# Kernel tuning notes

Measured on AMD Instinct MI355X. Metric: run time of the kernel, lower is better.

## Reference

```python
import jax, jax.numpy as jnp
import numpy as np

B, T, D = 8, 2048, 128        # batch, time, input_dim
C, CD = 8192, 128             # codebook_size, codebook_dim
COMMIT_W = 1.0                # commitment_weight
IN2Q_W = 0.25                 # input_to_quantize_commit_loss_weight
EPS = 1e-12


def setup_inputs() -> dict:
    key = jax.random.key(0)
    k = jax.random.split(key, 4)
    z = jax.random.normal(k[0], (B, T, D), jnp.float32)
    frozen_codebook = jax.random.normal(k[1], (C, CD), jnp.float32) * CD ** -0.5
    conv_v = jax.random.normal(k[2], (D, CD), jnp.float32) * CD ** -0.5  # weight-norm direction (1x1 conv weight squeezed)
    conv_g = jnp.linalg.norm(conv_v, axis=1)                             # weight-norm gain (torch init: g = ||v||)
    conv_b = jnp.zeros((D,), jnp.float32)
    return {"z": z, "frozen_codebook": frozen_codebook, "conv_v": conv_v,
            "conv_g": conv_g, "conv_b": conv_b}


def _implicit_codebook(fc, v, g, b):
    # weight-normed 1x1 conv == linear: w = g * v / ||v||_row ; out = fc @ w.T + b
    w = g[:, None] * v / jnp.linalg.norm(v, axis=1, keepdims=True)
    return fc @ w.T + b  # (C, D)


def _rotate_to(src, tgt):
    # rotation trick (Fifty et al.): Householder-style rotation, grads flow only through src
    sg = jax.lax.stop_gradient
    norm_src = jnp.linalg.norm(src, axis=-1, keepdims=True)
    norm_tgt = jnp.linalg.norm(tgt, axis=-1, keepdims=True)
    u = sg(src / jnp.maximum(norm_src, EPS))
    q = sg(tgt / jnp.maximum(norm_tgt, EPS))
    w = u + q
    w = sg(w / jnp.maximum(jnp.linalg.norm(w, axis=-1, keepdims=True), EPS))
    e = src
    rotated = (e
               - 2.0 * jnp.sum(e * w, -1, keepdims=True) * w
               + 2.0 * jnp.sum(e * u, -1, keepdims=True) * q)
    scale = sg(norm_tgt / jnp.maximum(norm_src, EPS))
    return rotated * scale


def reference(z, frozen_codebook, conv_v, conv_g, conv_b):
    sg = jax.lax.stop_gradient
    cb = _implicit_codebook(frozen_codebook, conv_v, conv_g, conv_b)  # (C, D)
    # squared euclidean distances -> same argmin as torch.cdist (p=2)
    d2 = (jnp.sum(z * z, -1, keepdims=True)
          - 2.0 * jnp.einsum('btd,cd->btc', z, cb)
          + jnp.sum(cb * cb, -1))                                     # (B, T, C)
    indices = jnp.argmin(d2, axis=-1)                                 # (B, T)
    z_q = cb[indices]                                                 # (B, T, D)
    commit = (jnp.mean((sg(z) - z_q) ** 2)
              + IN2Q_W * jnp.mean((z - sg(z_q)) ** 2))
    z_q = _rotate_to(z, z_q)
    return z_q, indices, commit * COMMIT_W
```

## Files before the change

kernel.cpp:

```cpp
#include <hip/hip_runtime.h>
#include <math.h>

#define NROWS 16384
#define DIM 128
#define NCODE 8192
#define EPSF 1e-12f

typedef float f32x4 __attribute__((ext_vector_type(4)));
typedef __bf16 bf16x8 __attribute__((ext_vector_type(8)));
typedef unsigned short u16x8 __attribute__((ext_vector_type(8)));

#define WS_NEED_BYTES 31571968ull

#define KT 12
#define TILE 4096

__device__ __forceinline__ float wave_sum(float x) {
#pragma unroll
  for (int off = 32; off > 0; off >>= 1) x += __shfl_xor(x, off, 64);
  return x;
}

__device__ __forceinline__ unsigned short f2bf(float x) {
  union { float f; unsigned int u; } v;
  v.f = x;
  unsigned int r = v.u + 0x7fffu + ((v.u >> 16) & 1u);
  return (unsigned short)(r >> 16);
}
__device__ __forceinline__ float bf2f(unsigned short h) {
  union { float f; unsigned int u; } v;
  v.u = ((unsigned int)h) << 16;
  return v.f;
}

__device__ __forceinline__ void gload_lds16(const unsigned short* g,
                                            unsigned short* l) {
  __builtin_amdgcn_global_load_lds(
      (const __attribute__((address_space(1))) void*)g,
      (__attribute__((address_space(3))) void*)l, 16, 0, 0);
}

__global__ void wprep_kernel(const float* __restrict__ v,
                             const float* __restrict__ g,
                             float* __restrict__ Wt) {
  const int d = blockIdx.x;
  const int lane = threadIdx.x;
  const float v0 = v[d * DIM + lane], v1 = v[d * DIM + lane + 64];
  const float ss = wave_sum(fmaf(v0, v0, v1 * v1));
  const float sc = g[d] / sqrtf(ss);
  Wt[lane * DIM + d] = v0 * sc;
  Wt[(lane + 64) * DIM + d] = v1 * sc;
}

__global__ __launch_bounds__(256, 2) void codebook_kernel(
    const float* __restrict__ fc, const float* __restrict__ Wt,
    const float* __restrict__ bias, float* __restrict__ cb,
    float* __restrict__ cnorm2, unsigned short* __restrict__ cbcat) {
  __shared__ float Ws[DIM][DIM];
  const int tid = threadIdx.x;
  for (int i = tid; i < 4096; i += 256)
    *(float4*)&Ws[0][i << 2] = *(const float4*)&Wt[i << 2];
  __syncthreads();

  const int lane = tid & 63, wid = tid >> 6;
  const int c0 = blockIdx.x * 16 + wid * 4;
  const float b0 = bias[lane], b1 = bias[lane + 64];

  for (int cc = 0; cc < 4; ++cc) {
    const int c = __builtin_amdgcn_readfirstlane(c0 + cc);
    float a0 = 0.f, a1 = 0.f;
    for (int k = 0; k < DIM; k += 4) {
      const float4 f4 = *(const float4*)&fc[c * DIM + k];
      a0 = fmaf(f4.x, Ws[k][lane], a0);
      a1 = fmaf(f4.x, Ws[k][lane + 64], a1);
      a0 = fmaf(f4.y, Ws[k + 1][lane], a0);
      a1 = fmaf(f4.y, Ws[k + 1][lane + 64], a1);
      a0 = fmaf(f4.z, Ws[k + 2][lane], a0);
      a1 = fmaf(f4.z, Ws[k + 2][lane + 64], a1);
      a0 = fmaf(f4.w, Ws[k + 3][lane], a0);
      a1 = fmaf(f4.w, Ws[k + 3][lane + 64], a1);
    }
    const float o0 = a0 + b0, o1 = a1 + b1;
    cb[c * DIM + lane] = o0;
    cb[c * DIM + lane + 64] = o1;
    const float ss = wave_sum(fmaf(o0, o0, o1 * o1));
    if (lane == 0) cnorm2[c] = ss;

    if (cbcat != nullptr) {
      const int ct = c >> 7, r = c & 127;
      const unsigned int swz = ((r >> 1) & 3) << 3;
      unsigned short* base = cbcat + (size_t)ct * (KT * TILE);
#pragma unroll
      for (int h = 0; h < 2; ++h) {
        const int d = lane + 64 * h;
        const float val = h ? o1 : o0;
        const unsigned short hi = f2bf(val);
        const unsigned short lo = f2bf(val - bf2f(hi));
        const int ktl = d >> 5;
        const int off = (r << 5) + ((d & 31) ^ swz);
        base[ktl * TILE + off] = hi;
        base[(4 + ktl) * TILE + off] = lo;
        base[(8 + ktl) * TILE + off] = hi;
      }
    }
  }
}

__global__ __launch_bounds__(256) void zprep_kernel(
    const float* __restrict__ z, unsigned short* __restrict__ zcat) {
  const int id = blockIdx.x * 256 + threadIdx.x;
  const int row = id / 48, s = id - row * 48;
  const int kt = s >> 2, s4 = s & 3;
  const int seg = kt >> 2;
  const int d0 = ((kt & 3) << 5) + (s4 << 3);
  const int r = row & 127, rb = row >> 7;
  const int slotsw = s4 ^ ((r >> 1) & 3);

  const float* zp = &z[(size_t)row * DIM + d0];
  u16x8 out;
#pragma unroll
  for (int i = 0; i < 8; ++i) {
    const float x = zp[i];
    unsigned short b = f2bf(x);
    if (seg == 2) b = f2bf(x - bf2f(b));
    out[i] = b;
  }
  *(u16x8*)&zcat[(size_t)(rb * KT + kt) * TILE + (r << 5) + (slotsw << 3)] =
      out;
}

__global__ __launch_bounds__(256, 4) void mfma_argmin_kernel(
    const unsigned short* __restrict__ zcat,
    const unsigned short* __restrict__ cbcat,
    const float* __restrict__ cnorm2, float* __restrict__ pval,
    int* __restrict__ pidx) {
  __shared__ __align__(16) unsigned short As[2][TILE];
  __shared__ __align__(16) unsigned short Bs[2][TILE];

  const int bid = blockIdx.x;
  const int swz = ((bid & 7) << 10) + (bid >> 3);
  const int rb = swz >> 6;
  const int ct = swz & 63;

  const int tid = threadIdx.x;
  const int lane = tid & 63, wid = tid >> 6;
  const int wr = wid >> 1, wc = wid & 1;
  const int l15 = lane & 15, lg = lane >> 4;

  const unsigned short* Ag = zcat + (size_t)rb * (KT * TILE);
  const unsigned short* Bg = cbcat + (size_t)ct * (KT * TILE);
  const int soff = (wid << 9) + (lane << 3);
  const int ldst = (wid << 9);

  f32x4 acc[4][4];
#pragma unroll
  for (int mi = 0; mi < 4; ++mi)
#pragma unroll
    for (int ni = 0; ni < 4; ++ni) acc[mi][ni] = f32x4{0.f, 0.f, 0.f, 0.f};

  int aoff[4], boff[4];
#pragma unroll
  for (int i = 0; i < 4; ++i) {
    const int ra = wr * 64 + i * 16 + l15;
    aoff[i] = (ra << 5) + ((lg << 3) ^ (((ra >> 1) & 3) << 3));
    const int rc = wc * 64 + i * 16 + l15;
    boff[i] = (rc << 5) + ((lg << 3) ^ (((rc >> 1) & 3) << 3));
  }

#pragma unroll
  for (int i = 0; i < 2; ++i) {
    gload_lds16(Ag + soff + (i << 11), &As[0][ldst + (i << 11) + (lane << 3)]);
    gload_lds16(Bg + soff + (i << 11), &Bs[0][ldst + (i << 11) + (lane << 3)]);
  }
  __syncthreads();

  for (int kt = 0; kt < KT; ++kt) {
    const int cur = kt & 1;
    if (kt + 1 < KT) {
      const unsigned short* ag = Ag + (kt + 1) * TILE;
      const unsigned short* bg = Bg + (kt + 1) * TILE;
#pragma unroll
      for (int i = 0; i < 2; ++i) {
        gload_lds16(ag + soff + (i << 11),
                    &As[cur ^ 1][ldst + (i << 11) + (lane << 3)]);
        gload_lds16(bg + soff + (i << 11),
                    &Bs[cur ^ 1][ldst + (i << 11) + (lane << 3)]);
      }
    }
    bf16x8 af[4], bfr[4];
#pragma unroll
    for (int i = 0; i < 4; ++i) af[i] = *(const bf16x8*)&As[cur][aoff[i]];
#pragma unroll
    for (int i = 0; i < 4; ++i) bfr[i] = *(const bf16x8*)&Bs[cur][boff[i]];
#pragma unroll
    for (int mi = 0; mi < 4; ++mi)
#pragma unroll
      for (int ni = 0; ni < 4; ++ni)
        acc[mi][ni] = __builtin_amdgcn_mfma_f32_16x16x32_bf16(
            af[mi], bfr[ni], acc[mi][ni], 0, 0, 0);
    __syncthreads();
  }

  float* exv = (float*)&As[0][0];
  int* exi = (int*)&Bs[0][0];

  float cn[4];
#pragma unroll
  for (int ni = 0; ni < 4; ++ni)
    cn[ni] = cnorm2[ct * 128 + wc * 64 + ni * 16 + l15];

#pragma unroll
  for (int mi = 0; mi < 4; ++mi) {
#pragma unroll
    for (int rg = 0; rg < 4; ++rg) {
      float bv = 3.4e38f;
      int bi = 0;
#pragma unroll
      for (int ni = 0; ni < 4; ++ni) {
        const float d = fmaf(-2.f, acc[mi][ni][rg], cn[ni]);
        if (d < bv) { bv = d; bi = ct * 128 + wc * 64 + ni * 16 + l15; }
      }
#pragma unroll
      for (int off = 1; off < 16; off <<= 1) {
        const float ov = __shfl_xor(bv, off, 64);
        const int oi = __shfl_xor(bi, off, 64);
        if (ov < bv || (ov == bv && oi < bi)) { bv = ov; bi = oi; }
      }
      if (l15 == 0) {
        const int rloc = wr * 64 + mi * 16 + (lg << 2) + rg;
        exv[wc * 128 + rloc] = bv;
        exi[wc * 128 + rloc] = bi;
      }
    }
  }
  __syncthreads();
  if (tid < 128) {
    const float v0 = exv[tid], v1 = exv[128 + tid];
    const int i0 = exi[tid], i1 = exi[128 + tid];
    const int row = rb * 128 + tid;
    const bool t = (v1 < v0);
    pval[(size_t)ct * NROWS + row] = t ? v1 : v0;
    pidx[(size_t)ct * NROWS + row] = t ? i1 : i0;
  }
}

__global__ __launch_bounds__(256, 1) void argmin_kernel(
    const float* __restrict__ z, const float* __restrict__ cb,
    const float* __restrict__ cnorm2, float* __restrict__ pval,
    int* __restrict__ pidx) {
  __shared__ float zs[128][DIM];
  __shared__ float cs[128][DIM];

  const int tid = threadIdx.x;
  const int rb = blockIdx.x >> 1;
  const int ch = blockIdx.x & 1;
  const int row0 = rb * 128;
  const int code0 = ch * (NCODE / 2);

  for (int i = tid; i < 128 * 32; i += 256) {
    const int r = i >> 5, f = i & 31;
    *(float4*)&zs[r][f << 2] = *(const float4*)&z[(row0 + r) * DIM + (f << 2)];
  }

  const int tx = tid & 15, ty = tid >> 4;
  const int sw = tx & 7;

  float best[8];
  int besti[8];
#pragma unroll
  for (int r = 0; r < 8; ++r) { best[r] = 3.4e38f; besti[r] = 0; }

  for (int cc = 0; cc < NCODE / 2; cc += 128) {
    __syncthreads();
    for (int i = tid; i < 128 * 32; i += 256) {
      const int r = i >> 5, f = i & 31;
      const int fg = f ^ (r & 7);
      *(float4*)&cs[r][f << 2] =
          *(const float4*)&cb[(code0 + cc + r) * DIM + (fg << 2)];
    }
    __syncthreads();

    float acc[8][8];
#pragma unroll
    for (int r = 0; r < 8; ++r)
#pragma unroll
      for (int j = 0; j < 8; ++j) acc[r][j] = 0.f;

    for (int k = 0; k < DIM; k += 4) {
      const int f = k >> 2;
      float4 zr[8], cr[8];
#pragma unroll
      for (int r = 0; r < 8; ++r) zr[r] = *(const float4*)&zs[ty + 16 * r][k];
      const int col = ((f ^ sw) << 2);
#pragma unroll
      for (int j = 0; j < 8; ++j) cr[j] = *(const float4*)&cs[tx + 16 * j][col];
#pragma unroll
      for (int r = 0; r < 8; ++r)
#pragma unroll
        for (int j = 0; j < 8; ++j) {
          acc[r][j] = fmaf(zr[r].x, cr[j].x, acc[r][j]);
          acc[r][j] = fmaf(zr[r].y, cr[j].y, acc[r][j]);
          acc[r][j] = fmaf(zr[r].z, cr[j].z, acc[r][j]);
          acc[r][j] = fmaf(zr[r].w, cr[j].w, acc[r][j]);
        }
    }

#pragma unroll
    for (int j = 0; j < 8; ++j) {
      const int code = code0 + cc + tx + 16 * j;
      const float cnv = cnorm2[code];
#pragma unroll
      for (int r = 0; r < 8; ++r) {
        const float s = fmaf(-2.f, acc[r][j], cnv);
        if (s < best[r]) { best[r] = s; besti[r] = code; }
      }
    }
  }

#pragma unroll
  for (int off = 1; off < 16; off <<= 1) {
#pragma unroll
    for (int r = 0; r < 8; ++r) {
      const float ov = __shfl_xor(best[r], off, 64);
      const int oi = __shfl_xor(besti[r], off, 64);
      if (ov < best[r] || (ov == best[r] && oi < besti[r])) {
        best[r] = ov;
        besti[r] = oi;
      }
    }
  }
  if (tx == 0) {
#pragma unroll
    for (int r = 0; r < 8; ++r) {
      const int row = row0 + ty + 16 * r;
      pval[(size_t)ch * NROWS + row] = best[r];
      pidx[(size_t)ch * NROWS + row] = besti[r];
    }
  }
}

__global__ __launch_bounds__(256) void rotate_kernel(
    const float* __restrict__ z, const float* __restrict__ cb,
    const float* __restrict__ pval, const int* __restrict__ pidx, int ntiles,
    float* __restrict__ out_zq, float* __restrict__ out_idx,
    float* __restrict__ partials) {
  const int tid = threadIdx.x;
  const int wid = tid >> 6, lane = tid & 63;
  const int row = blockIdx.x * 4 + wid;

  float bv = 3.4e38f;
  int bi = 0x7fffffff;
  if (lane < ntiles) {
    bv = pval[(size_t)lane * NROWS + row];
    bi = pidx[(size_t)lane * NROWS + row];
  }
#pragma unroll
  for (int off = 32; off > 0; off >>= 1) {
    const float ov = __shfl_xor(bv, off, 64);
    const int oi = __shfl_xor(bi, off, 64);
    if (ov < bv || (ov == bv && oi < bi)) { bv = ov; bi = oi; }
  }
  const int ci = bi;

  const float z0 = z[row * DIM + lane], z1 = z[row * DIM + lane + 64];
  const float c0 = cb[ci * DIM + lane], c1 = cb[ci * DIM + lane + 64];

  const float ns2 = wave_sum(fmaf(z0, z0, z1 * z1));
  const float nt2 = wave_sum(fmaf(c0, c0, c1 * c1));
  const float ns = sqrtf(ns2), nt = sqrtf(nt2);
  const float dns = fmaxf(ns, EPSF), dnt = fmaxf(nt, EPSF);
  const float u0 = z0 / dns, u1 = z1 / dns;
  const float q0 = c0 / dnt, q1 = c1 / dnt;
  float w0 = u0 + q0, w1 = u1 + q1;
  const float nw = sqrtf(wave_sum(fmaf(w0, w0, w1 * w1)));
  const float dnw = fmaxf(nw, EPSF);
  w0 /= dnw;
  w1 /= dnw;
  const float ew = wave_sum(fmaf(z0, w0, z1 * w1));
  const float eu = wave_sum(fmaf(z0, u0, z1 * u1));
  const float sc = nt / dns;
  const float o0 = (z0 - 2.f * ew * w0 + 2.f * eu * q0) * sc;
  const float o1 = (z1 - 2.f * ew * w1 + 2.f * eu * q1) * sc;
  out_zq[row * DIM + lane] = o0;
  out_zq[row * DIM + lane + 64] = o1;
  if (lane == 0) out_idx[row] = (float)ci;

  const float d0 = z0 - c0, d1 = z1 - c1;
  const float rsum = wave_sum(fmaf(d0, d0, d1 * d1));
  __shared__ float pr[4];
  if (lane == 0) pr[wid] = rsum;
  __syncthreads();
  if (tid == 0) partials[blockIdx.x] = (pr[0] + pr[1]) + (pr[2] + pr[3]);
}

__global__ void finalize_kernel(const float* __restrict__ partials,
                                float* __restrict__ out_commit) {
  __shared__ float red[256];
  const int tid = threadIdx.x;
  float s = 0.f;
  for (int i = tid; i < 4096; i += 256) s += partials[i];
  red[tid] = s;
  __syncthreads();
  for (int off = 128; off > 0; off >>= 1) {
    if (tid < off) red[tid] += red[tid + off];
    __syncthreads();
  }
  if (tid == 0) out_commit[0] = red[0] * (1.25f / ((float)NROWS * (float)DIM));
}

extern "C" void kernel_launch(void* const* d_in, const int* in_sizes, int n_in,
                              void* d_out, int out_size, void* d_ws,
                              size_t ws_size, hipStream_t stream) {
  const float* z = (const float*)d_in[0];
  const float* fc = (const float*)d_in[1];
  const float* conv_v = (const float*)d_in[2];
  const float* conv_g = (const float*)d_in[3];
  const float* conv_b = (const float*)d_in[4];
  float* out = (float*)d_out;

  float* ws = (float*)d_ws;
  float* cb = ws;
  float* cnorm2 = ws + 1048576;
  float* Wt = ws + 1056768;

  if (ws_size >= WS_NEED_BYTES) {
    unsigned short* zcat = (unsigned short*)(ws + 1073152);
    unsigned short* cbcat = (unsigned short*)(ws + 4218880);
    float* pval = ws + 5791744;
    int* pidx = (int*)(ws + 6840320);
    float* partials = ws + 7888896;

    wprep_kernel<<<DIM, 64, 0, stream>>>(conv_v, conv_g, Wt);
    codebook_kernel<<<NCODE / 16, 256, 0, stream>>>(fc, Wt, conv_b, cb, cnorm2,
                                                    cbcat);
    zprep_kernel<<<NROWS * 48 / 256, 256, 0, stream>>>(z, zcat);
    mfma_argmin_kernel<<<8192, 256, 0, stream>>>(zcat, cbcat, cnorm2, pval,
                                                 pidx);
    rotate_kernel<<<NROWS / 4, 256, 0, stream>>>(z, cb, pval, pidx, 64, out,
                                                 out + 2097152, partials);
    finalize_kernel<<<1, 256, 0, stream>>>(partials, out + 2113536);
  } else {
    float* pval = ws + 1073152;
    int* pidx = (int*)(ws + 1105920);
    float* partials = ws + 1138688;

    wprep_kernel<<<DIM, 64, 0, stream>>>(conv_v, conv_g, Wt);
    codebook_kernel<<<NCODE / 16, 256, 0, stream>>>(fc, Wt, conv_b, cb, cnorm2,
                                                    nullptr);
    argmin_kernel<<<256, 256, 0, stream>>>(z, cb, cnorm2, pval, pidx);
    rotate_kernel<<<NROWS / 4, 256, 0, stream>>>(z, cb, pval, pidx, 2, out,
                                                 out + 2097152, partials);
    finalize_kernel<<<1, 256, 0, stream>>>(partials, out + 2113536);
  }
}
```

Before: 221.5 us.

## Enlarge MFMA argmin tile to 256x256 with triple-buffered LDS pipeline

Raises the block tile of the split-bf16 distance GEMM from 128x128 to 256x256, using 512 threads with 8 waves each covering 128x64. The LDS pipeline goes from double to triple buffering with explicit vmcnt waits, a single barrier per k-step, and setprio around the MFMA burst. Block-to-tile mapping is regrouped by XCD for L2 locality, and the partial-argmin count per row halves to 32. The aim is more data reuse per load and fewer partial results, at the cost of more accumulator registers and lower occupancy.

```diff
diff --git a/kernel.cpp b/kernel.cpp
--- a/kernel.cpp
+++ b/kernel.cpp
@@ -13,7 +13,7 @@
 #define WS_NEED_BYTES 31571968ull
 
 #define KT 12
-#define TILE 4096
+#define TILE2 8192
 
 __device__ __forceinline__ float wave_sum(float x) {
 #pragma unroll
@@ -87,9 +87,9 @@
     if (lane == 0) cnorm2[c] = ss;
 
     if (cbcat != nullptr) {
-      const int ct = c >> 7, r = c & 127;
+      const int ct = c >> 8, r = c & 255;
       const unsigned int swz = ((r >> 1) & 3) << 3;
-      unsigned short* base = cbcat + (size_t)ct * (KT * TILE);
+      unsigned short* base = cbcat + (size_t)ct * (KT * TILE2);
 #pragma unroll
       for (int h = 0; h < 2; ++h) {
         const int d = lane + 64 * h;
@@ -98,9 +98,9 @@
         const unsigned short lo = f2bf(val - bf2f(hi));
         const int ktl = d >> 5;
         const int off = (r << 5) + ((d & 31) ^ swz);
-        base[ktl * TILE + off] = hi;
-        base[(4 + ktl) * TILE + off] = lo;
-        base[(8 + ktl) * TILE + off] = hi;
+        base[ktl * TILE2 + off] = hi;
+        base[(4 + ktl) * TILE2 + off] = lo;
+        base[(8 + ktl) * TILE2 + off] = hi;
       }
     }
   }
@@ -113,7 +113,7 @@
   const int kt = s >> 2, s4 = s & 3;
   const int seg = kt >> 2;
   const int d0 = ((kt & 3) << 5) + (s4 << 3);
-  const int r = row & 127, rb = row >> 7;
+  const int r = row & 255, rt = row >> 8;
   const int slotsw = s4 ^ ((r >> 1) & 3);
 
   const float* zp = &z[(size_t)row * DIM + d0];
@@ -125,92 +125,100 @@
     if (seg == 2) b = f2bf(x - bf2f(b));
     out[i] = b;
   }
-  *(u16x8*)&zcat[(size_t)(rb * KT + kt) * TILE + (r << 5) + (slotsw << 3)] =
+  *(u16x8*)&zcat[(size_t)(rt * KT + kt) * TILE2 + (r << 5) + (slotsw << 3)] =
       out;
 }
 
-__global__ __launch_bounds__(256, 4) void mfma_argmin_kernel(
+__global__ __launch_bounds__(512, 2) void mfma_argmin_kernel(
     const unsigned short* __restrict__ zcat,
     const unsigned short* __restrict__ cbcat,
     const float* __restrict__ cnorm2, float* __restrict__ pval,
     int* __restrict__ pidx) {
-  __shared__ __align__(16) unsigned short As[2][TILE];
-  __shared__ __align__(16) unsigned short Bs[2][TILE];
-
-  const int bid = blockIdx.x;
-  const int swz = ((bid & 7) << 10) + (bid >> 3);
-  const int rb = swz >> 6;
-  const int ct = swz & 63;
+  __shared__ __align__(16) unsigned short S[3 * 16384];
+
+  const int xcd = blockIdx.x & 7, idx = blockIdx.x >> 3;
+  const int rt = xcd * 8 + (idx & 7);
+  const int ct = idx >> 3;
 
   const int tid = threadIdx.x;
   const int lane = tid & 63, wid = tid >> 6;
-  const int wr = wid >> 1, wc = wid & 1;
+  const int wr = wid >> 2, wc = wid & 3;
   const int l15 = lane & 15, lg = lane >> 4;
-
-  const unsigned short* Ag = zcat + (size_t)rb * (KT * TILE);
-  const unsigned short* Bg = cbcat + (size_t)ct * (KT * TILE);
-  const int soff = (wid << 9) + (lane << 3);
-  const int ldst = (wid << 9);
-
-  f32x4 acc[4][4];
-#pragma unroll
-  for (int mi = 0; mi < 4; ++mi)
+  const int tid8 = tid * 8;
+
+  const unsigned short* Ag = zcat + (size_t)rt * (KT * TILE2);
+  const unsigned short* Bg = cbcat + (size_t)ct * (KT * TILE2);
+
+#define STAGE(ktile, buf)                                   \
+  do {                                                      \
+    const unsigned short* ag_ = Ag + (ktile)*TILE2 + tid8;  \
+    const unsigned short* bg_ = Bg + (ktile)*TILE2 + tid8;  \
+    unsigned short* la_ = &S[(buf)*16384 + tid8];           \
+    unsigned short* lb_ = &S[(buf)*16384 + 8192 + tid8];    \
+    gload_lds16(ag_, la_);                                  \
+    gload_lds16(ag_ + 4096, la_ + 4096);                    \
+    gload_lds16(bg_, lb_);                                  \
+    gload_lds16(bg_ + 4096, lb_ + 4096);                    \
+  } while (0)
+
+  f32x4 acc[8][4];
+#pragma unroll
+  for (int mi = 0; mi < 8; ++mi)
 #pragma unroll
     for (int ni = 0; ni < 4; ++ni) acc[mi][ni] = f32x4{0.f, 0.f, 0.f, 0.f};
 
-  int aoff[4], boff[4];
+  int aoff[8], boff[4];
+#pragma unroll
+  for (int i = 0; i < 8; ++i) {
+    const int ra = wr * 128 + i * 16 + l15;
+    aoff[i] = (ra << 5) + ((lg << 3) ^ (((ra >> 1) & 3) << 3));
+  }
 #pragma unroll
   for (int i = 0; i < 4; ++i) {
-    const int ra = wr * 64 + i * 16 + l15;
-    aoff[i] = (ra << 5) + ((lg << 3) ^ (((ra >> 1) & 3) << 3));
     const int rc = wc * 64 + i * 16 + l15;
-    boff[i] = (rc << 5) + ((lg << 3) ^ (((rc >> 1) & 3) << 3));
-  }
-
-#pragma unroll
-  for (int i = 0; i < 2; ++i) {
-    gload_lds16(Ag + soff + (i << 11), &As[0][ldst + (i << 11) + (lane << 3)]);
-    gload_lds16(Bg + soff + (i << 11), &Bs[0][ldst + (i << 11) + (lane << 3)]);
-  }
-  __syncthreads();
-
+    boff[i] = 8192 + (rc << 5) + ((lg << 3) ^ (((rc >> 1) & 3) << 3));
+  }
+
+  STAGE(0, 0);
+  STAGE(1, 1);
+
+#pragma unroll
   for (int kt = 0; kt < KT; ++kt) {
-    const int cur = kt & 1;
-    if (kt + 1 < KT) {
-      const unsigned short* ag = Ag + (kt + 1) * TILE;
-      const unsigned short* bg = Bg + (kt + 1) * TILE;
-#pragma unroll
-      for (int i = 0; i < 2; ++i) {
-        gload_lds16(ag + soff + (i << 11),
-                    &As[cur ^ 1][ldst + (i << 11) + (lane << 3)]);
-        gload_lds16(bg + soff + (i << 11),
-                    &Bs[cur ^ 1][ldst + (i << 11) + (lane << 3)]);
-      }
-    }
-    bf16x8 af[4], bfr[4];
-#pragma unroll
-    for (int i = 0; i < 4; ++i) af[i] = *(const bf16x8*)&As[cur][aoff[i]];
-#pragma unroll
-    for (int i = 0; i < 4; ++i) bfr[i] = *(const bf16x8*)&Bs[cur][boff[i]];
-#pragma unroll
-    for (int mi = 0; mi < 4; ++mi)
+    if (kt < KT - 1)
+      asm volatile("s_waitcnt vmcnt(4)" ::: "memory");
+    else
+      asm volatile("s_waitcnt vmcnt(0)" ::: "memory");
+    __builtin_amdgcn_s_barrier();
+    __builtin_amdgcn_sched_barrier(0);
+    if (kt + 2 < KT) STAGE(kt + 2, (kt + 2) % 3);
+    const int sb = (kt % 3) * 16384;
+    bf16x8 af[8], bfr[4];
+#pragma unroll
+    for (int i = 0; i < 8; ++i) af[i] = *(const bf16x8*)&S[sb + aoff[i]];
+#pragma unroll
+    for (int i = 0; i < 4; ++i) bfr[i] = *(const bf16x8*)&S[sb + boff[i]];
+    __builtin_amdgcn_s_setprio(1);
+#pragma unroll
+    for (int mi = 0; mi < 8; ++mi)
 #pragma unroll
       for (int ni = 0; ni < 4; ++ni)
         acc[mi][ni] = __builtin_amdgcn_mfma_f32_16x16x32_bf16(
             af[mi], bfr[ni], acc[mi][ni], 0, 0, 0);
-    __syncthreads();
-  }
-
-  float* exv = (float*)&As[0][0];
-  int* exi = (int*)&Bs[0][0];
+    __builtin_amdgcn_s_setprio(0);
+  }
+#undef STAGE
+  __syncthreads();
+
+  float* exv = (float*)&S[0];
+  int* exi = (int*)&S[2048];
 
   float cn[4];
 #pragma unroll
   for (int ni = 0; ni < 4; ++ni)
-    cn[ni] = cnorm2[ct * 128 + wc * 64 + ni * 16 + l15];
-
-#pragma unroll
-  for (int mi = 0; mi < 4; ++mi) {
+    cn[ni] = cnorm2[ct * 256 + wc * 64 + ni * 16 + l15];
+
+#pragma unroll
+  for (int mi = 0; mi < 8; ++mi) {
 #pragma unroll
     for (int rg = 0; rg < 4; ++rg) {
       float bv = 3.4e38f;
@@ -218,7 +226,7 @@
 #pragma unroll
       for (int ni = 0; ni < 4; ++ni) {
         const float d = fmaf(-2.f, acc[mi][ni][rg], cn[ni]);
-        if (d < bv) { bv = d; bi = ct * 128 + wc * 64 + ni * 16 + l15; }
+        if (d < bv) { bv = d; bi = ct * 256 + wc * 64 + ni * 16 + l15; }
       }
 #pragma unroll
       for (int off = 1; off < 16; off <<= 1) {
@@ -227,20 +235,24 @@
         if (ov < bv || (ov == bv && oi < bi)) { bv = ov; bi = oi; }
       }
       if (l15 == 0) {
-        const int rloc = wr * 64 + mi * 16 + (lg << 2) + rg;
-        exv[wc * 128 + rloc] = bv;
-        exi[wc * 128 + rloc] = bi;
+        const int rloc = wr * 128 + mi * 16 + (lg << 2) + rg;
+        exv[wc * 256 + rloc] = bv;
+        exi[wc * 256 + rloc] = bi;
       }
     }
   }
   __syncthreads();
-  if (tid < 128) {
-    const float v0 = exv[tid], v1 = exv[128 + tid];
-    const int i0 = exi[tid], i1 = exi[128 + tid];
-    const int row = rb * 128 + tid;
-    const bool t = (v1 < v0);
-    pval[(size_t)ct * NROWS + row] = t ? v1 : v0;
-    pidx[(size_t)ct * NROWS + row] = t ? i1 : i0;
+  if (tid < 256) {
+    float bv = exv[tid];
+    int bi = exi[tid];
+#pragma unroll
+    for (int w = 1; w < 4; ++w) {
+      const float v = exv[w * 256 + tid];
+      if (v < bv) { bv = v; bi = exi[w * 256 + tid]; }
+    }
+    const int row = rt * 256 + tid;
+    pval[(size_t)ct * NROWS + row] = bv;
+    pidx[(size_t)ct * NROWS + row] = bi;
   }
 }
 
@@ -434,9 +446,9 @@
     codebook_kernel<<<NCODE / 16, 256, 0, stream>>>(fc, Wt, conv_b, cb, cnorm2,
                                                     cbcat);
     zprep_kernel<<<NROWS * 48 / 256, 256, 0, stream>>>(z, zcat);
-    mfma_argmin_kernel<<<8192, 256, 0, stream>>>(zcat, cbcat, cnorm2, pval,
+    mfma_argmin_kernel<<<2048, 512, 0, stream>>>(zcat, cbcat, cnorm2, pval,
                                                  pidx);
-    rotate_kernel<<<NROWS / 4, 256, 0, stream>>>(z, cb, pval, pidx, 64, out,
+    rotate_kernel<<<NROWS / 4, 256, 0, stream>>>(z, cb, pval, pidx, 32, out,
                                                  out + 2097152, partials);
     finalize_kernel<<<1, 256, 0, stream>>>(partials, out + 2113536);
   } else {
```

After: 247.9 us. 1.12x slower.

## Widen MFMA argmin tile to 128x256 with 8 waves, single-buffered LDS

Applied to the files above, without the earlier changes.

The MFMA distance/argmin kernel now uses 512-thread blocks that each cover 128 rows by 256 codes, so every loaded z tile is reused across twice as many codes and the number of per-row partial results drops from 64 to 32. The codebook tile layout and the rotate kernel's partial count are updated to match. LDS double buffering is removed in favour of one buffer with a sync before and after each k-step load, which may expose global-load latency. The block-to-XCD mapping is also changed so row tiles are grouped per XCD.

```diff
diff --git a/kernel.cpp b/kernel.cpp
--- a/kernel.cpp
+++ b/kernel.cpp
@@ -13,7 +13,8 @@
 #define WS_NEED_BYTES 31571968ull
 
 #define KT 12
-#define TILE 4096
+#define TILEA 4096
+#define TILEB 8192
 
 __device__ __forceinline__ float wave_sum(float x) {
 #pragma unroll
@@ -87,9 +88,9 @@
     if (lane == 0) cnorm2[c] = ss;
 
     if (cbcat != nullptr) {
-      const int ct = c >> 7, r = c & 127;
+      const int ct = c >> 8, r = c & 255;
       const unsigned int swz = ((r >> 1) & 3) << 3;
-      unsigned short* base = cbcat + (size_t)ct * (KT * TILE);
+      unsigned short* base = cbcat + (size_t)ct * (KT * TILEB);
 #pragma unroll
       for (int h = 0; h < 2; ++h) {
         const int d = lane + 64 * h;
@@ -98,9 +99,9 @@
         const unsigned short lo = f2bf(val - bf2f(hi));
         const int ktl = d >> 5;
         const int off = (r << 5) + ((d & 31) ^ swz);
-        base[ktl * TILE + off] = hi;
-        base[(4 + ktl) * TILE + off] = lo;
-        base[(8 + ktl) * TILE + off] = hi;
+        base[ktl * TILEB + off] = hi;
+        base[(4 + ktl) * TILEB + off] = lo;
+        base[(8 + ktl) * TILEB + off] = hi;
       }
     }
   }
@@ -113,7 +114,7 @@
   const int kt = s >> 2, s4 = s & 3;
   const int seg = kt >> 2;
   const int d0 = ((kt & 3) << 5) + (s4 << 3);
-  const int r = row & 127, rb = row >> 7;
+  const int r = row & 127, rt = row >> 7;
   const int slotsw = s4 ^ ((r >> 1) & 3);
 
   const float* zp = &z[(size_t)row * DIM + d0];
@@ -125,32 +126,29 @@
     if (seg == 2) b = f2bf(x - bf2f(b));
     out[i] = b;
   }
-  *(u16x8*)&zcat[(size_t)(rb * KT + kt) * TILE + (r << 5) + (slotsw << 3)] =
+  *(u16x8*)&zcat[(size_t)(rt * KT + kt) * TILEA + (r << 5) + (slotsw << 3)] =
       out;
 }
 
-__global__ __launch_bounds__(256, 4) void mfma_argmin_kernel(
+__global__ __launch_bounds__(512, 4) void mfma_argmin_kernel(
     const unsigned short* __restrict__ zcat,
     const unsigned short* __restrict__ cbcat,
     const float* __restrict__ cnorm2, float* __restrict__ pval,
     int* __restrict__ pidx) {
-  __shared__ __align__(16) unsigned short As[2][TILE];
-  __shared__ __align__(16) unsigned short Bs[2][TILE];
-
-  const int bid = blockIdx.x;
-  const int swz = ((bid & 7) << 10) + (bid >> 3);
-  const int rb = swz >> 6;
-  const int ct = swz & 63;
+  __shared__ __align__(16) unsigned short S[TILEA + TILEB];
+
+  const int xcd = blockIdx.x & 7, idx = blockIdx.x >> 3;
+  const int rt = xcd * 16 + (idx & 15);
+  const int ct = idx >> 4;
 
   const int tid = threadIdx.x;
   const int lane = tid & 63, wid = tid >> 6;
-  const int wr = wid >> 1, wc = wid & 1;
+  const int wr = wid >> 2, wc = wid & 3;
   const int l15 = lane & 15, lg = lane >> 4;
-
-  const unsigned short* Ag = zcat + (size_t)rb * (KT * TILE);
-  const unsigned short* Bg = cbcat + (size_t)ct * (KT * TILE);
-  const int soff = (wid << 9) + (lane << 3);
-  const int ldst = (wid << 9);
+  const int tid8 = tid * 8;
+
+  const unsigned short* Ag = zcat + (size_t)rt * (KT * TILEA);
+  const unsigned short* Bg = cbcat + (size_t)ct * (KT * TILEB);
 
   f32x4 acc[4][4];
 #pragma unroll
@@ -162,52 +160,39 @@
 #pragma unroll
   for (int i = 0; i < 4; ++i) {
     const int ra = wr * 64 + i * 16 + l15;
-    aoff[i] = (ra << 5) + ((lg << 3) ^ (((ra >> 1) & 3) << 3));
+    aoff[i] = (ra << 5) + ((lg ^ ((ra >> 1) & 3)) << 3);
     const int rc = wc * 64 + i * 16 + l15;
-    boff[i] = (rc << 5) + ((lg << 3) ^ (((rc >> 1) & 3) << 3));
-  }
-
-#pragma unroll
-  for (int i = 0; i < 2; ++i) {
-    gload_lds16(Ag + soff + (i << 11), &As[0][ldst + (i << 11) + (lane << 3)]);
-    gload_lds16(Bg + soff + (i << 11), &Bs[0][ldst + (i << 11) + (lane << 3)]);
-  }
-  __syncthreads();
+    boff[i] = TILEA + (rc << 5) + ((lg ^ ((rc >> 1) & 3)) << 3);
+  }
 
   for (int kt = 0; kt < KT; ++kt) {
-    const int cur = kt & 1;
-    if (kt + 1 < KT) {
-      const unsigned short* ag = Ag + (kt + 1) * TILE;
-      const unsigned short* bg = Bg + (kt + 1) * TILE;
-#pragma unroll
-      for (int i = 0; i < 2; ++i) {
-        gload_lds16(ag + soff + (i << 11),
-                    &As[cur ^ 1][ldst + (i << 11) + (lane << 3)]);
-        gload_lds16(bg + soff + (i << 11),
-                    &Bs[cur ^ 1][ldst + (i << 11) + (lane << 3)]);
-      }
-    }
+    __syncthreads();
+    gload_lds16(Ag + kt * TILEA + tid8, &S[tid8]);
+    gload_lds16(Bg + kt * TILEB + tid8, &S[TILEA + tid8]);
+    gload_lds16(Bg + kt * TILEB + 4096 + tid8, &S[TILEA + 4096 + tid8]);
+    __syncthreads();
+
     bf16x8 af[4], bfr[4];
 #pragma unroll
-    for (int i = 0; i < 4; ++i) af[i] = *(const bf16x8*)&As[cur][aoff[i]];
-#pragma unroll
-    for (int i = 0; i < 4; ++i) bfr[i] = *(const bf16x8*)&Bs[cur][boff[i]];
+    for (int i = 0; i < 4; ++i) af[i] = *(const bf16x8*)&S[aoff[i]];
+#pragma unroll
+    for (int i = 0; i < 4; ++i) bfr[i] = *(const bf16x8*)&S[boff[i]];
 #pragma unroll
     for (int mi = 0; mi < 4; ++mi)
 #pragma unroll
       for (int ni = 0; ni < 4; ++ni)
         acc[mi][ni] = __builtin_amdgcn_mfma_f32_16x16x32_bf16(
             af[mi], bfr[ni], acc[mi][ni], 0, 0, 0);
-    __syncthreads();
-  }
-
-  float* exv = (float*)&As[0][0];
-  int* exi = (int*)&Bs[0][0];
+  }
+  __syncthreads();
+
+  float* exv = (float*)&S[0];
+  int* exi = (int*)&S[2048];
 
   float cn[4];
 #pragma unroll
   for (int ni = 0; ni < 4; ++ni)
-    cn[ni] = cnorm2[ct * 128 + wc * 64 + ni * 16 + l15];
+    cn[ni] = cnorm2[ct * 256 + wc * 64 + ni * 16 + l15];
 
 #pragma unroll
   for (int mi = 0; mi < 4; ++mi) {
@@ -218,7 +203,7 @@
 #pragma unroll
       for (int ni = 0; ni < 4; ++ni) {
         const float d = fmaf(-2.f, acc[mi][ni][rg], cn[ni]);
-        if (d < bv) { bv = d; bi = ct * 128 + wc * 64 + ni * 16 + l15; }
+        if (d < bv) { bv = d; bi = ct * 256 + wc * 64 + ni * 16 + l15; }
       }
 #pragma unroll
       for (int off = 1; off < 16; off <<= 1) {
@@ -235,12 +220,16 @@
   }
   __syncthreads();
   if (tid < 128) {
-    const float v0 = exv[tid], v1 = exv[128 + tid];
-    const int i0 = exi[tid], i1 = exi[128 + tid];
-    const int row = rb * 128 + tid;
-    const bool t = (v1 < v0);
-    pval[(size_t)ct * NROWS + row] = t ? v1 : v0;
-    pidx[(size_t)ct * NROWS + row] = t ? i1 : i0;
+    float bv = exv[tid];
+    int bi = exi[tid];
+#pragma unroll
+    for (int w = 1; w < 4; ++w) {
+      const float v = exv[w * 128 + tid];
+      if (v < bv) { bv = v; bi = exi[w * 128 + tid]; }
+    }
+    const int row = rt * 128 + tid;
+    pval[(size_t)ct * NROWS + row] = bv;
+    pidx[(size_t)ct * NROWS + row] = bi;
   }
 }
 
@@ -434,9 +423,9 @@
     codebook_kernel<<<NCODE / 16, 256, 0, stream>>>(fc, Wt, conv_b, cb, cnorm2,
                                                     cbcat);
     zprep_kernel<<<NROWS * 48 / 256, 256, 0, stream>>>(z, zcat);
-    mfma_argmin_kernel<<<8192, 256, 0, stream>>>(zcat, cbcat, cnorm2, pval,
+    mfma_argmin_kernel<<<4096, 512, 0, stream>>>(zcat, cbcat, cnorm2, pval,
                                                  pidx);
-    rotate_kernel<<<NROWS / 4, 256, 0, stream>>>(z, cb, pval, pidx, 64, out,
+    rotate_kernel<<<NROWS / 4, 256, 0, stream>>>(z, cb, pval, pidx, 32, out,
                                                  out + 2097152, partials);
     finalize_kernel<<<1, 256, 0, stream>>>(partials, out + 2113536);
   } else {
```

Measured after the change: 212.8 us. -3.9%, faster.
